# Optimization experiments

Hardware: AMD Instinct MI355X
Metric: run time of the kernel (lower is better)

Reference implementation:

```python
import jax, jax.numpy as jnp
import numpy as np

K = 8  # kernel_size
COUT = 512


def setup_inputs() -> dict:
    key = jax.random.key(0)
    k1, k2, k3 = jax.random.split(key, 3)
    B, CIN, L = 8, 512, 2048
    x = jax.random.normal(k1, (B, CIN, L), dtype=jnp.float32)
    # nn.Linear(CIN, COUT*K) weight, scaled like kaiming-uniform-ish init
    W = jax.random.normal(k2, (COUT * K, CIN), dtype=jnp.float32) * (1.0 / np.sqrt(CIN))
    b = jax.random.normal(k3, (COUT,), dtype=jnp.float32)
    return {"x": x, "W": W, "b": b}


def reference(x, W, b):
    # x: (B, Cin, L); W: (Cout*K, Cin) with row layout j = k*Cout + co; b: (Cout,)
    B, Cin, L = x.shape
    # pointwise linear expand: (B, Cout*K, L)
    z = jnp.einsum('bcl,oc->bol', x, W)
    z = z.reshape(B, K, COUT, L)  # k-major channel layout
    # causal overlap-add fold: y[b,co,t] = sum_k z[b,k,co,t-k]
    y = z[:, 0]
    for k in range(1, K):  # small fixed kernel-size loop
        y = y.at[:, :, k:].add(z[:, k, :, : L - k])
    return y + b[None, :, None]
```

## Files before the change

kernel.cpp:

```cpp
#include <hip/hip_runtime.h>
#include <hip/hip_bf16.h>
#include <cstdint>
#include <cstddef>

#define CIN   512
#define COUT  512
#define LLEN  2048
#define BATCH 8
#define KTAP  8
#define LPAD  (LLEN + 8)

typedef __bf16 bf16x8_t __attribute__((ext_vector_type(8)));
typedef float  f32x4_t  __attribute__((ext_vector_type(4)));
typedef unsigned short u16x8_t __attribute__((ext_vector_type(8)));

__device__ __forceinline__ unsigned short f2bf(float f) {
  __bf16 h = (__bf16)f;
  return __builtin_bit_cast(unsigned short, h);
}

__device__ __forceinline__ void gl2lds16(unsigned short* lds, const unsigned short* g) {
  __builtin_amdgcn_global_load_lds(
      (const __attribute__((address_space(1))) unsigned int*)g,
      (__attribute__((address_space(3))) unsigned int*)lds,
      16, 0, 0);
}

__global__ __launch_bounds__(256) void prepass_kernel(
    const float* __restrict__ x, unsigned short* __restrict__ xtp,
    const float4* __restrict__ W, u16x8_t* __restrict__ Wb) {
  const int bid = blockIdx.x;
  const int t   = threadIdx.x;

  if (bid >= 2048) {
    int idx = (bid - 2048) * 256 + t;
    float4 a = W[idx * 2], b = W[idx * 2 + 1];
    u16x8_t o;
    o[0] = f2bf(a.x); o[1] = f2bf(a.y); o[2] = f2bf(a.z); o[3] = f2bf(a.w);
    o[4] = f2bf(b.x); o[5] = f2bf(b.y); o[6] = f2bf(b.z); o[7] = f2bf(b.w);
    Wb[idx] = o;
    return;
  }

  __shared__ float tile[64][65];
  const int b  = bid >> 8;
  const int c0 = ((bid >> 5) & 7) * 64;
  const int l0 = (bid & 31) * 64;

  if ((bid & 31) == 0 && t < 64) {
    unsigned short* hp = xtp + ((size_t)b * LPAD + (t >> 3)) * CIN + c0 + (t & 7) * 8;
    *(u16x8_t*)hp = (u16x8_t){0, 0, 0, 0, 0, 0, 0, 0};
  }

  {
    const int cr = t >> 2;
    const int lv = (t & 3) * 16;
    const float* src = x + ((size_t)b * CIN + c0 + cr) * LLEN + l0 + lv;
#pragma unroll
    for (int i = 0; i < 4; ++i) {
      float4 v = *(const float4*)(src + 4 * i);
      tile[cr][lv + 4 * i + 0] = v.x;
      tile[cr][lv + 4 * i + 1] = v.y;
      tile[cr][lv + 4 * i + 2] = v.z;
      tile[cr][lv + 4 * i + 3] = v.w;
    }
  }
  __syncthreads();
  {
    const int l    = t >> 2;
    const int cseg = (t & 3) * 16;
    unsigned short ov[16];
#pragma unroll
    for (int u = 0; u < 16; ++u) ov[u] = f2bf(tile[cseg + u][l]);
    unsigned short* dst = xtp + ((size_t)b * LPAD + 8 + l0 + l) * CIN + c0 + cseg;
    *(u16x8_t*)dst       = *(const u16x8_t*)&ov[0];
    *(u16x8_t*)(dst + 8) = *(const u16x8_t*)&ov[8];
  }
}


__global__ __launch_bounds__(512) void conv_gemm_kernel(
    const unsigned short* __restrict__ Wb,
    const unsigned short* __restrict__ xtp,
    const float* __restrict__ bias,
    float* __restrict__ y)
{
  __shared__ __align__(16) unsigned short As[2][256 * 64];
  __shared__ __align__(16) unsigned short Bs[2][136 * 64];

  const int t    = threadIdx.x;
  const int lane = t & 63;
  const int wid  = t >> 6;
  const int wm   = wid & 3;
  const int wn   = wid >> 2;
  const int l0   = blockIdx.x * 128;
  const int o0   = blockIdx.y * 256;
  const int b    = blockIdx.z;

  const int quad = lane >> 4;
  const int lrow = lane & 15;

  f32x4_t acc[4][4];
#pragma unroll
  for (int i = 0; i < 4; ++i)
#pragma unroll
    for (int j = 0; j < 4; ++j)
      acc[i][j] = (f32x4_t){0.f, 0.f, 0.f, 0.f};

  const int srow    = t >> 3;
  const int schunk  = (t & 7) ^ (srow & 7);
  const int lds_off = t * 8;

  const unsigned short* xb = xtp + (size_t)b * LPAD * CIN;

  auto stage_A = [&](int kk, int buf) {
    const unsigned short* asrc =
        Wb + (size_t)((kk & 7) * COUT + o0 + srow) * CIN + (kk >> 3) * 64 + schunk * 8;
#pragma unroll
    for (int rd = 0; rd < 4; ++rd)
      gl2lds16(&As[buf][0] + lds_off + rd * 4096, asrc + (size_t)rd * 64 * CIN);
  };
  auto stage_B = [&](int ct, int buf) {
    const int c0 = ct * 64;
    const unsigned short* src = xb + (size_t)(l0 + srow) * CIN + c0 + schunk * 8;
#pragma unroll
    for (int rd = 0; rd < 2; ++rd)
      gl2lds16(&Bs[buf][0] + lds_off + rd * 4096, src + (size_t)rd * 64 * CIN);
    if (t < 64) {
      const int r2  = 128 + (t >> 3);
      const int ch2 = (t & 7) ^ (r2 & 7);
      gl2lds16(&Bs[buf][0] + 128 * 64 + t * 8,
               xb + (size_t)(l0 + r2) * CIN + c0 + ch2 * 8);
    }
  };

  stage_B(0, 0);
  stage_A(0, 0);
  __syncthreads();

#pragma unroll 1
  for (int kk = 0; kk < 64; ++kk) {
    const int k  = kk & 7;
    const int ct = kk >> 3;
    if (kk + 1 < 64) stage_A(kk + 1, (kk + 1) & 1);
    if (k == 7 && ct + 1 < 8) stage_B(ct + 1, (ct + 1) & 1);

    const unsigned short* Ac = &As[kk & 1][0];
    const unsigned short* Bc = &Bs[ct & 1][0];
#pragma unroll
    for (int h = 0; h < 2; ++h) {
      bf16x8_t af[4], bfr[4];
#pragma unroll
      for (int i = 0; i < 4; ++i) {
        int row  = wm * 64 + i * 16 + lrow;
        int slot = (h * 4 + quad) ^ (row & 7);
        af[i] = *(const bf16x8_t*)(Ac + row * 64 + slot * 8);
      }
#pragma unroll
      for (int j = 0; j < 4; ++j) {
        int row  = (8 - k) + wn * 64 + j * 16 + lrow;
        int slot = (h * 4 + quad) ^ (row & 7);
        bfr[j] = *(const bf16x8_t*)(Bc + row * 64 + slot * 8);
      }
      __builtin_amdgcn_s_setprio(1);
#pragma unroll
      for (int i = 0; i < 4; ++i)
#pragma unroll
        for (int j = 0; j < 4; ++j)
          acc[i][j] = __builtin_amdgcn_mfma_f32_16x16x32_bf16(af[i], bfr[j], acc[i][j], 0, 0, 0);
      __builtin_amdgcn_s_setprio(0);
    }
    __syncthreads();
  }

#pragma unroll
  for (int i = 0; i < 4; ++i) {
    const int o_base = o0 + wm * 64 + i * 16 + quad * 4;
    const float4 bv = *(const float4*)(bias + o_base);
    const float bvr[4] = {bv.x, bv.y, bv.z, bv.w};
#pragma unroll
    for (int j = 0; j < 4; ++j) {
      const int l = l0 + wn * 64 + j * 16 + lrow;
#pragma unroll
      for (int r = 0; r < 4; ++r) {
        y[((size_t)b * COUT + o_base + r) * LLEN + l] = acc[i][j][r] + bvr[r];
      }
    }
  }
}


extern "C" void kernel_launch(void* const* d_in, const int* in_sizes, int n_in,
                              void* d_out, int out_size, void* d_ws, size_t ws_size,
                              hipStream_t stream) {
  const float* x    = (const float*)d_in[0];
  const float* W    = (const float*)d_in[1];
  const float* bias = (const float*)d_in[2];
  float* y          = (float*)d_out;

  unsigned short* xtp = (unsigned short*)d_ws;
  unsigned short* Wb  = (unsigned short*)((char*)d_ws +
                        (size_t)BATCH * LPAD * CIN * sizeof(unsigned short));

  prepass_kernel<<<2048 + 1024, 256, 0, stream>>>(
      x, xtp, (const float4*)W, (u16x8_t*)Wb);
  conv_gemm_kernel<<<dim3(LLEN / 128, COUT / 256, BATCH), 512, 0, stream>>>(
      Wb, xtp, bias, y);
}
```

Baseline: 169.7 us.

## Halve output tile and split K across warp groups with LDS reduction

The GEMM tile shrinks from 256 to 128 output channels per block, and the eight waves are split into two groups that each take half of every 64-wide reduction chunk. The partial accumulators are then summed through LDS before the output is written. This doubles the grid and cuts LDS per block, aiming for more resident blocks and better CU utilisation. In exchange, each B tile is reloaded twice as often per output, and the end-of-kernel reduction adds a sync and extra LDS traffic.

```diff
diff --git a/kernel.cpp b/kernel.cpp
--- a/kernel.cpp
+++ b/kernel.cpp
@@ -79,26 +79,29 @@
 }
 
 
-__global__ __launch_bounds__(512) void conv_gemm_kernel(
+__global__ __launch_bounds__(512, 4) void conv_gemm_kernel(
     const unsigned short* __restrict__ Wb,
     const unsigned short* __restrict__ xtp,
     const float* __restrict__ bias,
     float* __restrict__ y)
 {
-  __shared__ __align__(16) unsigned short As[2][256 * 64];
-  __shared__ __align__(16) unsigned short Bs[2][136 * 64];
+  __shared__ __align__(16) unsigned char smem[67584];
 
   const int t    = threadIdx.x;
   const int lane = t & 63;
   const int wid  = t >> 6;
-  const int wm   = wid & 3;
-  const int wn   = wid >> 2;
+  const int wm   = wid & 1;
+  const int wn   = (wid >> 1) & 1;
+  const int hg   = wid >> 2;
   const int l0   = blockIdx.x * 128;
-  const int o0   = blockIdx.y * 256;
+  const int o0   = blockIdx.y * 128;
   const int b    = blockIdx.z;
 
   const int quad = lane >> 4;
   const int lrow = lane & 15;
+
+  unsigned short* AsBuf = (unsigned short*)smem;
+  unsigned short* BsBuf = (unsigned short*)(smem + 32768);
 
   f32x4_t acc[4][4];
 #pragma unroll
@@ -117,19 +120,19 @@
     const unsigned short* asrc =
         Wb + (size_t)((kk & 7) * COUT + o0 + srow) * CIN + (kk >> 3) * 64 + schunk * 8;
 #pragma unroll
-    for (int rd = 0; rd < 4; ++rd)
-      gl2lds16(&As[buf][0] + lds_off + rd * 4096, asrc + (size_t)rd * 64 * CIN);
+    for (int rd = 0; rd < 2; ++rd)
+      gl2lds16(AsBuf + buf * 8192 + lds_off + rd * 4096, asrc + (size_t)rd * 64 * CIN);
   };
   auto stage_B = [&](int ct, int buf) {
     const int c0 = ct * 64;
     const unsigned short* src = xb + (size_t)(l0 + srow) * CIN + c0 + schunk * 8;
 #pragma unroll
     for (int rd = 0; rd < 2; ++rd)
-      gl2lds16(&Bs[buf][0] + lds_off + rd * 4096, src + (size_t)rd * 64 * CIN);
+      gl2lds16(BsBuf + buf * 8704 + lds_off + rd * 4096, src + (size_t)rd * 64 * CIN);
     if (t < 64) {
       const int r2  = 128 + (t >> 3);
       const int ch2 = (t & 7) ^ (r2 & 7);
-      gl2lds16(&Bs[buf][0] + 128 * 64 + t * 8,
+      gl2lds16(BsBuf + buf * 8704 + 128 * 64 + t * 8,
                xb + (size_t)(l0 + r2) * CIN + c0 + ch2 * 8);
     }
   };
@@ -145,45 +148,56 @@
     if (kk + 1 < 64) stage_A(kk + 1, (kk + 1) & 1);
     if (k == 7 && ct + 1 < 8) stage_B(ct + 1, (ct + 1) & 1);
 
-    const unsigned short* Ac = &As[kk & 1][0];
-    const unsigned short* Bc = &Bs[ct & 1][0];
-#pragma unroll
-    for (int h = 0; h < 2; ++h) {
-      bf16x8_t af[4], bfr[4];
-#pragma unroll
-      for (int i = 0; i < 4; ++i) {
-        int row  = wm * 64 + i * 16 + lrow;
-        int slot = (h * 4 + quad) ^ (row & 7);
-        af[i] = *(const bf16x8_t*)(Ac + row * 64 + slot * 8);
-      }
+    const unsigned short* Ac = AsBuf + (kk & 1) * 8192;
+    const unsigned short* Bc = BsBuf + (ct & 1) * 8704;
+    bf16x8_t af[4], bfr[4];
+#pragma unroll
+    for (int i = 0; i < 4; ++i) {
+      int row  = wm * 64 + i * 16 + lrow;
+      int slot = (hg * 4 + quad) ^ (row & 7);
+      af[i] = *(const bf16x8_t*)(Ac + row * 64 + slot * 8);
+    }
+#pragma unroll
+    for (int j = 0; j < 4; ++j) {
+      int row  = (8 - k) + wn * 64 + j * 16 + lrow;
+      int slot = (hg * 4 + quad) ^ (row & 7);
+      bfr[j] = *(const bf16x8_t*)(Bc + row * 64 + slot * 8);
+    }
+    __builtin_amdgcn_s_setprio(1);
+#pragma unroll
+    for (int i = 0; i < 4; ++i)
+#pragma unroll
+      for (int j = 0; j < 4; ++j)
+        acc[i][j] = __builtin_amdgcn_mfma_f32_16x16x32_bf16(af[i], bfr[j], acc[i][j], 0, 0, 0);
+    __builtin_amdgcn_s_setprio(0);
+    __syncthreads();
+  }
+
+  float* red = (float*)smem + (size_t)(wn * 2 + wm) * 4096;
+  if (hg == 1) {
+#pragma unroll
+    for (int i = 0; i < 4; ++i)
+#pragma unroll
+      for (int j = 0; j < 4; ++j)
+#pragma unroll
+        for (int r = 0; r < 4; ++r)
+          red[((i * 4 + j) * 4 + r) * 64 + lane] = acc[i][j][r];
+  }
+  __syncthreads();
+  if (hg == 0) {
+#pragma unroll
+    for (int i = 0; i < 4; ++i) {
+      const int o_base = o0 + wm * 64 + i * 16 + quad * 4;
+      const float4 bv = *(const float4*)(bias + o_base);
+      const float bvr[4] = {bv.x, bv.y, bv.z, bv.w};
 #pragma unroll
       for (int j = 0; j < 4; ++j) {
-        int row  = (8 - k) + wn * 64 + j * 16 + lrow;
-        int slot = (h * 4 + quad) ^ (row & 7);
-        bfr[j] = *(const bf16x8_t*)(Bc + row * 64 + slot * 8);
-      }
-      __builtin_amdgcn_s_setprio(1);
-#pragma unroll
-      for (int i = 0; i < 4; ++i)
-#pragma unroll
-        for (int j = 0; j < 4; ++j)
-          acc[i][j] = __builtin_amdgcn_mfma_f32_16x16x32_bf16(af[i], bfr[j], acc[i][j], 0, 0, 0);
-      __builtin_amdgcn_s_setprio(0);
-    }
-    __syncthreads();
-  }
-
-#pragma unroll
-  for (int i = 0; i < 4; ++i) {
-    const int o_base = o0 + wm * 64 + i * 16 + quad * 4;
-    const float4 bv = *(const float4*)(bias + o_base);
-    const float bvr[4] = {bv.x, bv.y, bv.z, bv.w};
-#pragma unroll
-    for (int j = 0; j < 4; ++j) {
-      const int l = l0 + wn * 64 + j * 16 + lrow;
-#pragma unroll
-      for (int r = 0; r < 4; ++r) {
-        y[((size_t)b * COUT + o_base + r) * LLEN + l] = acc[i][j][r] + bvr[r];
+        const int l = l0 + wn * 64 + j * 16 + lrow;
+#pragma unroll
+        for (int r = 0; r < 4; ++r) {
+          float v = acc[i][j][r] + red[((i * 4 + j) * 4 + r) * 64 + lane];
+          y[((size_t)b * COUT + o_base + r) * LLEN + l] = v + bvr[r];
+        }
       }
     }
   }
@@ -204,6 +218,6 @@
 
   prepass_kernel<<<2048 + 1024, 256, 0, stream>>>(
       x, xtp, (const float4*)W, (u16x8_t*)Wb);
-  conv_gemm_kernel<<<dim3(LLEN / 128, COUT / 256, BATCH), 512, 0, stream>>>(
+  conv_gemm_kernel<<<dim3(LLEN / 128, COUT / 128, BATCH), 512, 0, stream>>>(
       Wb, xtp, bias, y);
 }
```

Result: faster. 147.8 us (-12.9%).
